# Kernel optimization log

Measured on AMD Instinct MI355X. Metric: run time of the kernel, lower is better.

## Reference

```python
import jax, jax.numpy as jnp
import numpy as np


def setup_inputs() -> dict:
    key = jax.random.key(0)
    kq, kk, kv = jax.random.split(key, 3)
    B, S, D = 16, 2048, 128
    q = jax.random.normal(kq, (B, S, D), dtype=jnp.float32)
    k = jax.random.normal(kk, (B, S, D), dtype=jnp.float32)
    v = jax.random.normal(kv, (B, S, D), dtype=jnp.float32)
    return {"q": q, "k": k, "v": v}


def reference(q, k, v):
    # q: (B, Sq, Dk), k: (B, Skv, Dk), v: (B, Skv, Dv)
    d_k = k.shape[-1]
    scale = 1.0 / jnp.sqrt(jnp.asarray(d_k, dtype=q.dtype))
    scores = jnp.einsum("bqd,bkd->bqk", q, k) * scale  # (B, Sq, Skv)
    # causal mask: strictly-upper-triangular positions set to -inf (mask=True in init)
    Sq = q.shape[-2]
    causal = jnp.triu(jnp.ones((Sq, Sq), dtype=bool), k=1)
    scores = jnp.where(causal, -jnp.inf, scores)
    attn = jax.nn.softmax(scores, axis=-1)
    return jnp.einsum("bqk,bkd->bqd", attn, v)
```

## Files before the change

kernel.cpp:

```cpp
#include <hip/hip_runtime.h>
#include <hip/hip_bf16.h>

typedef __bf16 bf16;
typedef bf16 bf16x8 __attribute__((ext_vector_type(8)));
typedef bf16 bf16x4 __attribute__((ext_vector_type(4)));
typedef float f32x4 __attribute__((ext_vector_type(4)));

#define DHEAD 128
#define SCALE 0.08838834764831843f
#define LOG2E 1.4426950408889634f

__global__ __launch_bounds__(256) void fa_fwd(
    const float* __restrict__ Q, const float* __restrict__ K,
    const float* __restrict__ V, float* __restrict__ O, int S)
{
  const int bid = blockIdx.x;
  const int pr  = bid & 255;
  const int hb  = bid >> 8;
  const int b   = pr & 15;
  const int jj  = pr >> 4;
  const int qt  = hb ? jj : (31 - jj);

  const int tid  = threadIdx.x;
  const int wave = tid >> 6;
  const int lane = tid & 63;
  const int lr   = lane & 15;
  const int lg   = lane >> 4;

  __shared__ bf16 Ks[2][32][136];
  __shared__ bf16 Vt[2][DHEAD][56];
  __shared__ bf16 Ps[4][16][40];

  const size_t bo = (size_t)b * S * DHEAD;
  const float* Qb = Q + bo + (size_t)qt * 64 * DHEAD;
  const float* Kb = K + bo;
  const float* Vb = V + bo;
  const int wrow0 = qt * 64 + wave * 16;

  const int srow = tid >> 5;
  const int d4   = (tid & 31) << 2;
  const int vsw  = (d4 >> 4) & 3;

  bf16x8 qf[4];
  {
    const float* qr = Qb + (size_t)(wave * 16 + lr) * DHEAD;
    #pragma unroll
    for (int c = 0; c < 4; ++c) {
      const float4 u0 = *reinterpret_cast<const float4*>(qr + c * 32 + lg * 8);
      const float4 u1 = *reinterpret_cast<const float4*>(qr + c * 32 + lg * 8 + 4);
      bf16x8 f;
      f[0] = (bf16)u0.x; f[1] = (bf16)u0.y; f[2] = (bf16)u0.z; f[3] = (bf16)u0.w;
      f[4] = (bf16)u1.x; f[5] = (bf16)u1.y; f[6] = (bf16)u1.z; f[7] = (bf16)u1.w;
      qf[c] = f;
    }
  }

  f32x4 oacc[8];
  #pragma unroll
  for (int i = 0; i < 8; ++i) oacc[i] = (f32x4){0.f, 0.f, 0.f, 0.f};
  float m[4], l[4];
  #pragma unroll
  for (int r = 0; r < 4; ++r) { m[r] = -__builtin_inff(); l[r] = 0.f; }

  const int nt = 2 * (qt + 1);
  float4 kreg[4], vreg[4];

  auto load_tile = [&](int kc) {
    #pragma unroll
    for (int i = 0; i < 4; ++i) {
      kreg[i] = *reinterpret_cast<const float4*>(Kb + (size_t)(kc + 8 * i + srow) * DHEAD + d4);
      vreg[i] = *reinterpret_cast<const float4*>(Vb + (size_t)(kc + 8 * i + srow) * DHEAD + d4);
    }
  };
  auto write_tile = [&](int buf) {
    #pragma unroll
    for (int i = 0; i < 4; ++i) {
      const int kv = 8 * i + srow;
      bf16x4 kp;
      kp[0] = (bf16)kreg[i].x; kp[1] = (bf16)kreg[i].y;
      kp[2] = (bf16)kreg[i].z; kp[3] = (bf16)kreg[i].w;
      *reinterpret_cast<bf16x4*>(&Ks[buf][kv][d4]) = kp;
      const int col = (kv & 7) | (((kv >> 3) ^ vsw) << 3);
      Vt[buf][d4 + 0][col] = (bf16)vreg[i].x;
      Vt[buf][d4 + 1][col] = (bf16)vreg[i].y;
      Vt[buf][d4 + 2][col] = (bf16)vreg[i].z;
      Vt[buf][d4 + 3][col] = (bf16)vreg[i].w;
    }
  };

  load_tile(0);
  write_tile(0);

  int cur = 0;
  for (int t = 0; t < nt; ++t) {
    if (t + 1 < nt) load_tile((t + 1) * 32);
    __syncthreads();

    const int kc = t * 32;
    if (kc <= wrow0 + 15) {
      f32x4 s0 = {0.f, 0.f, 0.f, 0.f}, s1 = {0.f, 0.f, 0.f, 0.f};
      __builtin_amdgcn_s_setprio(1);
      #pragma unroll
      for (int c = 0; c < 4; ++c) {
        const bf16x8 kf0 = *reinterpret_cast<const bf16x8*>(&Ks[cur][lr][c * 32 + lg * 8]);
        const bf16x8 kf1 = *reinterpret_cast<const bf16x8*>(&Ks[cur][16 + lr][c * 32 + lg * 8]);
        s0 = __builtin_amdgcn_mfma_f32_16x16x32_bf16(qf[c], kf0, s0, 0, 0, 0);
        s1 = __builtin_amdgcn_mfma_f32_16x16x32_bf16(qf[c], kf1, s1, 0, 0, 0);
      }
      __builtin_amdgcn_s_setprio(0);

      const bool need_mask = (kc + 31 > wrow0);
      float mt[4];
      #pragma unroll
      for (int r = 0; r < 4; ++r) {
        float x0 = s0[r] * SCALE;
        float x1 = s1[r] * SCALE;
        if (need_mask) {
          const int qrow = wrow0 + lg * 4 + r;
          if (kc + lr > qrow)      x0 = -__builtin_inff();
          if (kc + 16 + lr > qrow) x1 = -__builtin_inff();
        }
        s0[r] = x0; s1[r] = x1;
        float v = fmaxf(x0, x1);
        v = fmaxf(v, __shfl_xor(v, 1));
        v = fmaxf(v, __shfl_xor(v, 2));
        v = fmaxf(v, __shfl_xor(v, 4));
        v = fmaxf(v, __shfl_xor(v, 8));
        mt[r] = v;
      }

      float alpha[4];
      #pragma unroll
      for (int r = 0; r < 4; ++r) {
        const float mn = fmaxf(m[r], mt[r]);
        alpha[r] = __builtin_exp2f((m[r] - mn) * LOG2E);
        m[r] = mn;
      }
      #pragma unroll
      for (int r = 0; r < 4; ++r) {
        const float p0 = __builtin_exp2f((s0[r] - m[r]) * LOG2E);
        const float p1 = __builtin_exp2f((s1[r] - m[r]) * LOG2E);
        float ls = p0 + p1;
        ls += __shfl_xor(ls, 1);
        ls += __shfl_xor(ls, 2);
        ls += __shfl_xor(ls, 4);
        ls += __shfl_xor(ls, 8);
        l[r] = l[r] * alpha[r] + ls;
        Ps[wave][lg * 4 + r][lr]      = (bf16)p0;
        Ps[wave][lg * 4 + r][16 + lr] = (bf16)p1;
      }
      #pragma unroll
      for (int ds = 0; ds < 8; ++ds) {
        #pragma unroll
        for (int r = 0; r < 4; ++r) oacc[ds][r] *= alpha[r];
      }

      const bf16x8 pf = *reinterpret_cast<const bf16x8*>(&Ps[wave][lr][lg * 8]);
      __builtin_amdgcn_s_setprio(1);
      #pragma unroll
      for (int ds = 0; ds < 8; ++ds) {
        const int d  = ds * 16 + lr;
        const int sg = (lg ^ (ds & 3)) << 3;
        const bf16x8 vf = *reinterpret_cast<const bf16x8*>(&Vt[cur][d][sg]);
        oacc[ds] = __builtin_amdgcn_mfma_f32_16x16x32_bf16(pf, vf, oacc[ds], 0, 0, 0);
      }
      __builtin_amdgcn_s_setprio(0);
    }

    if (t + 1 < nt) write_tile(cur ^ 1);
    cur ^= 1;
  }

  float* Ob = O + bo + (size_t)(qt * 64 + wave * 16) * DHEAD;
  float inv[4];
  #pragma unroll
  for (int r = 0; r < 4; ++r) inv[r] = 1.0f / l[r];
  #pragma unroll
  for (int ds = 0; ds < 8; ++ds) {
    #pragma unroll
    for (int r = 0; r < 4; ++r) {
      Ob[(size_t)(lg * 4 + r) * DHEAD + ds * 16 + lr] = oacc[ds][r] * inv[r];
    }
  }
}

extern "C" void kernel_launch(void* const* d_in, const int* in_sizes, int n_in,
                              void* d_out, int out_size, void* d_ws, size_t ws_size,
                              hipStream_t stream) {
  const float* q = (const float*)d_in[0];
  const float* k = (const float*)d_in[1];
  const float* v = (const float*)d_in[2];
  float* o = (float*)d_out;

  const int B = 16;
  const int S = in_sizes[0] / (B * DHEAD);

  dim3 grid(512);
  dim3 block(256);
  fa_fwd<<<grid, block, 0, stream>>>(q, k, v, o, S);
}
```

Baseline: 191.6 us.

## Transpose QK^T MFMA, lazy rescale softmax, packed V transpose, deeper prefetch

Result: faster. 162.7 us (-15.1%).

```diff
diff --git a/kernel.cpp b/kernel.cpp
--- a/kernel.cpp
+++ b/kernel.cpp
@@ -7,18 +7,25 @@
 typedef float f32x4 __attribute__((ext_vector_type(4)));
 
 #define DHEAD 128
-#define SCALE 0.08838834764831843f
-#define LOG2E 1.4426950408889634f
+#define SCL2 0.1275500811965365f
+#define NINF (-__builtin_inff())
+
+__device__ __forceinline__ unsigned pk2(float a, float b) {
+  bf16 x = (bf16)a, y = (bf16)b;
+  unsigned short ux = __builtin_bit_cast(unsigned short, x);
+  unsigned short uy = __builtin_bit_cast(unsigned short, y);
+  return ((unsigned)uy << 16) | (unsigned)ux;
+}
 
 __global__ __launch_bounds__(256) void fa_fwd(
     const float* __restrict__ Q, const float* __restrict__ K,
     const float* __restrict__ V, float* __restrict__ O, int S)
 {
   const int bid = blockIdx.x;
-  const int pr  = bid & 255;
+  const int prb = bid & 255;
   const int hb  = bid >> 8;
-  const int b   = pr & 15;
-  const int jj  = pr >> 4;
+  const int b   = prb & 15;
+  const int jj  = prb >> 4;
   const int qt  = hb ? jj : (31 - jj);
 
   const int tid  = threadIdx.x;
@@ -28,7 +35,7 @@
   const int lg   = lane >> 4;
 
   __shared__ bf16 Ks[2][32][136];
-  __shared__ bf16 Vt[2][DHEAD][56];
+  __shared__ bf16 Vt[2][DHEAD][40];
   __shared__ bf16 Ps[4][16][40];
 
   const size_t bo = (size_t)b * S * DHEAD;
@@ -37,9 +44,10 @@
   const float* Vb = V + bo;
   const int wrow0 = qt * 64 + wave * 16;
 
-  const int srow = tid >> 5;
-  const int d4   = (tid & 31) << 2;
-  const int vsw  = (d4 >> 4) & 3;
+  const int j   = tid & 31;
+  const int prw = tid >> 5;
+  const int d4  = j << 2;
+  const int Gw  = (j >> 1) & 3;
 
   bf16x8 qf[4];
   {
@@ -58,43 +66,53 @@
   f32x4 oacc[8];
   #pragma unroll
   for (int i = 0; i < 8; ++i) oacc[i] = (f32x4){0.f, 0.f, 0.f, 0.f};
-  float m[4], l[4];
-  #pragma unroll
-  for (int r = 0; r < 4; ++r) { m[r] = -__builtin_inff(); l[r] = 0.f; }
+  float m = NINF, l = 0.f;
 
   const int nt = 2 * (qt + 1);
-  float4 kreg[4], vreg[4];
+  float4 kA[2], kB[2], vA[2], vB[2];
 
   auto load_tile = [&](int kc) {
     #pragma unroll
-    for (int i = 0; i < 4; ++i) {
-      kreg[i] = *reinterpret_cast<const float4*>(Kb + (size_t)(kc + 8 * i + srow) * DHEAD + d4);
-      vreg[i] = *reinterpret_cast<const float4*>(Vb + (size_t)(kc + 8 * i + srow) * DHEAD + d4);
+    for (int ps = 0; ps < 2; ++ps) {
+      const int kv = kc + 2 * (prw + 8 * ps);
+      const float* kp = Kb + (size_t)kv * DHEAD + d4;
+      const float* vp = Vb + (size_t)kv * DHEAD + d4;
+      kA[ps] = *reinterpret_cast<const float4*>(kp);
+      kB[ps] = *reinterpret_cast<const float4*>(kp + DHEAD);
+      vA[ps] = *reinterpret_cast<const float4*>(vp);
+      vB[ps] = *reinterpret_cast<const float4*>(vp + DHEAD);
     }
   };
   auto write_tile = [&](int buf) {
     #pragma unroll
-    for (int i = 0; i < 4; ++i) {
-      const int kv = 8 * i + srow;
-      bf16x4 kp;
-      kp[0] = (bf16)kreg[i].x; kp[1] = (bf16)kreg[i].y;
-      kp[2] = (bf16)kreg[i].z; kp[3] = (bf16)kreg[i].w;
-      *reinterpret_cast<bf16x4*>(&Ks[buf][kv][d4]) = kp;
-      const int col = (kv & 7) | (((kv >> 3) ^ vsw) << 3);
-      Vt[buf][d4 + 0][col] = (bf16)vreg[i].x;
-      Vt[buf][d4 + 1][col] = (bf16)vreg[i].y;
-      Vt[buf][d4 + 2][col] = (bf16)vreg[i].z;
-      Vt[buf][d4 + 3][col] = (bf16)vreg[i].w;
+    for (int ps = 0; ps < 2; ++ps) {
+      const int kvp = prw + 8 * ps;
+      bf16x4 ka, kb;
+      ka[0] = (bf16)kA[ps].x; ka[1] = (bf16)kA[ps].y;
+      ka[2] = (bf16)kA[ps].z; ka[3] = (bf16)kA[ps].w;
+      kb[0] = (bf16)kB[ps].x; kb[1] = (bf16)kB[ps].y;
+      kb[2] = (bf16)kB[ps].z; kb[3] = (bf16)kB[ps].w;
+      *reinterpret_cast<bf16x4*>(&Ks[buf][2 * kvp][d4])     = ka;
+      *reinterpret_cast<bf16x4*>(&Ks[buf][2 * kvp + 1][d4]) = kb;
+      const int pS = kvp ^ (Gw << 2);
+      const float* fa = &vA[ps].x;
+      const float* fb = &vB[ps].x;
+      #pragma unroll
+      for (int c = 0; c < 4; ++c) {
+        *reinterpret_cast<unsigned*>(&Vt[buf][d4 + c][2 * pS]) = pk2(fa[c], fb[c]);
+      }
     }
   };
 
   load_tile(0);
   write_tile(0);
+  if (nt > 1) load_tile(32);
 
   int cur = 0;
   for (int t = 0; t < nt; ++t) {
-    if (t + 1 < nt) load_tile((t + 1) * 32);
     __syncthreads();
+    if (t + 1 < nt) write_tile(cur ^ 1);
+    if (t + 2 < nt) load_tile((t + 2) * 32);
 
     const int kc = t * 32;
     if (kc <= wrow0 + 15) {
@@ -104,82 +122,79 @@
       for (int c = 0; c < 4; ++c) {
         const bf16x8 kf0 = *reinterpret_cast<const bf16x8*>(&Ks[cur][lr][c * 32 + lg * 8]);
         const bf16x8 kf1 = *reinterpret_cast<const bf16x8*>(&Ks[cur][16 + lr][c * 32 + lg * 8]);
-        s0 = __builtin_amdgcn_mfma_f32_16x16x32_bf16(qf[c], kf0, s0, 0, 0, 0);
-        s1 = __builtin_amdgcn_mfma_f32_16x16x32_bf16(qf[c], kf1, s1, 0, 0, 0);
+        s0 = __builtin_amdgcn_mfma_f32_16x16x32_bf16(kf0, qf[c], s0, 0, 0, 0);
+        s1 = __builtin_amdgcn_mfma_f32_16x16x32_bf16(kf1, qf[c], s1, 0, 0, 0);
       }
       __builtin_amdgcn_s_setprio(0);
 
-      const bool need_mask = (kc + 31 > wrow0);
-      float mt[4];
+      const int qg = wrow0 + lr;
+      float x0[4], x1[4];
+      if (kc + 31 > wrow0) {
+        #pragma unroll
+        for (int r = 0; r < 4; ++r) {
+          x0[r] = (kc + 4 * lg + r      > qg) ? NINF : s0[r] * SCL2;
+          x1[r] = (kc + 16 + 4 * lg + r > qg) ? NINF : s1[r] * SCL2;
+        }
+      } else {
+        #pragma unroll
+        for (int r = 0; r < 4; ++r) { x0[r] = s0[r] * SCL2; x1[r] = s1[r] * SCL2; }
+      }
+      float tm = NINF;
+      #pragma unroll
+      for (int r = 0; r < 4; ++r) tm = fmaxf(tm, fmaxf(x0[r], x1[r]));
+      tm = fmaxf(tm, __shfl_xor(tm, 16));
+      tm = fmaxf(tm, __shfl_xor(tm, 32));
+
+      if (!__all(tm <= m + 8.0f)) {
+        const float mn = fmaxf(m, tm);
+        const float al = __builtin_exp2f(m - mn);
+        m = mn; l *= al;
+        #pragma unroll
+        for (int r = 0; r < 4; ++r) {
+          const float ar = __shfl(al, 4 * lg + r);
+          #pragma unroll
+          for (int ds = 0; ds < 8; ++ds) oacc[ds][r] *= ar;
+        }
+      }
+
+      float p0[4], p1[4];
+      float ts = 0.f;
       #pragma unroll
       for (int r = 0; r < 4; ++r) {
-        float x0 = s0[r] * SCALE;
-        float x1 = s1[r] * SCALE;
-        if (need_mask) {
-          const int qrow = wrow0 + lg * 4 + r;
-          if (kc + lr > qrow)      x0 = -__builtin_inff();
-          if (kc + 16 + lr > qrow) x1 = -__builtin_inff();
-        }
-        s0[r] = x0; s1[r] = x1;
-        float v = fmaxf(x0, x1);
-        v = fmaxf(v, __shfl_xor(v, 1));
-        v = fmaxf(v, __shfl_xor(v, 2));
-        v = fmaxf(v, __shfl_xor(v, 4));
-        v = fmaxf(v, __shfl_xor(v, 8));
-        mt[r] = v;
-      }
-
-      float alpha[4];
-      #pragma unroll
-      for (int r = 0; r < 4; ++r) {
-        const float mn = fmaxf(m[r], mt[r]);
-        alpha[r] = __builtin_exp2f((m[r] - mn) * LOG2E);
-        m[r] = mn;
-      }
-      #pragma unroll
-      for (int r = 0; r < 4; ++r) {
-        const float p0 = __builtin_exp2f((s0[r] - m[r]) * LOG2E);
-        const float p1 = __builtin_exp2f((s1[r] - m[r]) * LOG2E);
-        float ls = p0 + p1;
-        ls += __shfl_xor(ls, 1);
-        ls += __shfl_xor(ls, 2);
-        ls += __shfl_xor(ls, 4);
-        ls += __shfl_xor(ls, 8);
-        l[r] = l[r] * alpha[r] + ls;
-        Ps[wave][lg * 4 + r][lr]      = (bf16)p0;
-        Ps[wave][lg * 4 + r][16 + lr] = (bf16)p1;
-      }
-      #pragma unroll
-      for (int ds = 0; ds < 8; ++ds) {
-        #pragma unroll
-        for (int r = 0; r < 4; ++r) oacc[ds][r] *= alpha[r];
-      }
+        p0[r] = __builtin_exp2f(x0[r] - m);
+        p1[r] = __builtin_exp2f(x1[r] - m);
+        ts += p0[r] + p1[r];
+      }
+      ts += __shfl_xor(ts, 16);
+      ts += __shfl_xor(ts, 32);
+      l += ts;
+
+      *reinterpret_cast<unsigned*>(&Ps[wave][lr][4 * lg])          = pk2(p0[0], p0[1]);
+      *reinterpret_cast<unsigned*>(&Ps[wave][lr][4 * lg + 2])      = pk2(p0[2], p0[3]);
+      *reinterpret_cast<unsigned*>(&Ps[wave][lr][16 + 4 * lg])     = pk2(p1[0], p1[1]);
+      *reinterpret_cast<unsigned*>(&Ps[wave][lr][16 + 4 * lg + 2]) = pk2(p1[2], p1[3]);
 
       const bf16x8 pf = *reinterpret_cast<const bf16x8*>(&Ps[wave][lr][lg * 8]);
       __builtin_amdgcn_s_setprio(1);
       #pragma unroll
       for (int ds = 0; ds < 8; ++ds) {
-        const int d  = ds * 16 + lr;
-        const int sg = (lg ^ (ds & 3)) << 3;
-        const bf16x8 vf = *reinterpret_cast<const bf16x8*>(&Vt[cur][d][sg]);
+        const int G = (2 * ds + (lr >> 3)) & 3;
+        const bf16x8 vf = *reinterpret_cast<const bf16x8*>(&Vt[cur][ds * 16 + lr][8 * (lg ^ G)]);
         oacc[ds] = __builtin_amdgcn_mfma_f32_16x16x32_bf16(pf, vf, oacc[ds], 0, 0, 0);
       }
       __builtin_amdgcn_s_setprio(0);
     }
-
-    if (t + 1 < nt) write_tile(cur ^ 1);
     cur ^= 1;
   }
 
+  const float linv = 1.0f / l;
   float* Ob = O + bo + (size_t)(qt * 64 + wave * 16) * DHEAD;
-  float inv[4];
   #pragma unroll
-  for (int r = 0; r < 4; ++r) inv[r] = 1.0f / l[r];
-  #pragma unroll
-  for (int ds = 0; ds < 8; ++ds) {
-    #pragma unroll
-    for (int r = 0; r < 4; ++r) {
-      Ob[(size_t)(lg * 4 + r) * DHEAD + ds * 16 + lr] = oacc[ds][r] * inv[r];
+  for (int r = 0; r < 4; ++r) {
+    const float ir = __shfl(linv, 4 * lg + r);
+    #pragma unroll
+    for (int ds = 0; ds < 8; ++ds) {
+      Ob[(size_t)(4 * lg + r) * DHEAD + ds * 16 + lr] = oacc[ds][r] * ir;
     }
   }
 }
```
